# Kernel optimization log

Measured on AMD Instinct MI355X. Metric: run time of the kernel, lower is better.

Reference implementation:

```python
import jax, jax.numpy as jnp
import numpy as np

B, S, H, NH = 4, 2048, 1024, 16
HS = H // NH


def setup_inputs() -> dict:
    key = jax.random.key(0)
    ks = jax.random.split(key, 9)
    s = 0.02
    return {
        "x": jax.random.normal(ks[0], (B, S, H), dtype=jnp.float32),
        "Wq": jax.random.normal(ks[1], (H, H), dtype=jnp.float32) * s,
        "bq": jnp.zeros((H,), dtype=jnp.float32),
        "Wk": jax.random.normal(ks[2], (H, H), dtype=jnp.float32) * s,
        "bk": jnp.zeros((H,), dtype=jnp.float32),
        "Wv": jax.random.normal(ks[3], (H, H), dtype=jnp.float32) * s,
        "bv": jnp.zeros((H,), dtype=jnp.float32),
        "Wp": jax.random.normal(ks[4], (H, H), dtype=jnp.float32) * s,
        "bp": jnp.zeros((H,), dtype=jnp.float32),
    }


def _split_heads(t):
    # [B,S,H] -> [B,NH,S,HS]
    b, s, _ = t.shape
    return t.reshape(b, s, NH, HS).swapaxes(1, 2)


def reference(x, Wq, bq, Wk, bk, Wv, bv, Wp, bp):
    # torch Linear: y = x @ W.T + b
    q = _split_heads(x @ Wq.T + bq)
    k = _split_heads(x @ Wk.T + bk)
    v = _split_heads(x @ Wv.T + bv)
    scale = 1.0 / np.sqrt(HS).astype(np.float32)
    scores = jnp.einsum('bhqd,bhkd->bhqk', q, k) * scale  # [B,NH,S,S]
    n_pos = scores.shape[2]
    causal = jnp.arange(n_pos)[None, :] <= jnp.arange(n_pos)[:, None]
    mask_value = jnp.finfo(scores.dtype).min
    scores = jnp.where(causal, scores, mask_value)
    attn_w = jax.nn.softmax(scores, axis=-1)
    # dropout is identity in eval mode
    attn = jnp.einsum('bhqk,bhkd->bhqd', attn_w, v)
    attn = attn.swapaxes(1, 2).reshape(x.shape[0], n_pos, H)
    return attn @ Wp.T + bp
```

## Files before the change

kernel.cpp:

```cpp
#include <hip/hip_runtime.h>

#define B_ 4
#define S_ 2048
#define H_ 1024
#define NH_ 16
#define HS_ 64
#define SG_ (B_*S_)

typedef __bf16 bf16x8 __attribute__((ext_vector_type(8)));
typedef __bf16 bf16x4 __attribute__((ext_vector_type(4)));
typedef float  f32x4  __attribute__((ext_vector_type(4)));

#define M3(a,b,c) fmaxf(fmaxf((a),(b)),(c))

__device__ __forceinline__ void gload16(const void* g, void* l) {
    __builtin_amdgcn_global_load_lds(
        (const __attribute__((address_space(1))) void*)g,
        (__attribute__((address_space(3))) void*)l,
        16, 0, 0);
}

__global__ void cvt_f32_bf16(const float* __restrict__ in, __bf16* __restrict__ out, int n4) {
    int i = blockIdx.x * blockDim.x + threadIdx.x;
    if (i >= n4) return;
    float4 v = reinterpret_cast<const float4*>(in)[i];
    bf16x4 o;
    o[0] = (__bf16)v.x; o[1] = (__bf16)v.y; o[2] = (__bf16)v.z; o[3] = (__bf16)v.w;
    reinterpret_cast<bf16x4*>(out)[i] = o;
}

__global__ void cvt_w4(const float* __restrict__ w0, const float* __restrict__ w1,
                       const float* __restrict__ w2, const float* __restrict__ w3,
                       __bf16* __restrict__ o0, __bf16* __restrict__ o1,
                       __bf16* __restrict__ o2, __bf16* __restrict__ o3, int n4) {
    int i = blockIdx.x * blockDim.x + threadIdx.x;
    if (i >= n4) return;
    const float* in; __bf16* out;
    switch (blockIdx.y) {
        case 0: in = w0; out = o0; break;
        case 1: in = w1; out = o1; break;
        case 2: in = w2; out = o2; break;
        default: in = w3; out = o3; break;
    }
    float4 v = reinterpret_cast<const float4*>(in)[i];
    bf16x4 o;
    o[0] = (__bf16)v.x; o[1] = (__bf16)v.y; o[2] = (__bf16)v.z; o[3] = (__bf16)v.w;
    reinterpret_cast<bf16x4*>(out)[i] = o;
}

__device__ __forceinline__ void store_tile(const f32x4& acc, long mbase, long nbase, int lane,
                                           const float* __restrict__ bias, void* __restrict__ out,
                                           long N, int out_f32, int bias_row) {
    const int r16 = lane & 15, kg = lane >> 4;
    const long col = nbase + r16;
    const float bc = bias_row ? 0.f : bias[col];
#pragma unroll
    for (int r = 0; r < 4; ++r) {
        const long row = mbase + kg * 4 + r;
        const float v = acc[r] + (bias_row ? bias[row] : bc);
        if (out_f32) ((float*)out)[row * N + col] = v;
        else         ((__bf16*)out)[row * N + col] = (__bf16)v;
    }
}

__global__ __launch_bounds__(256) void gemm128(
    const __bf16* __restrict__ A, const __bf16* __restrict__ W,
    const float* __restrict__ bias, void* __restrict__ out,
    int M, int N, int K, int out_f32, int bias_row)
{
    __shared__ __bf16 sA[2][128][64];
    __shared__ __bf16 sB[2][128][64];
    const int lane = threadIdx.x & 63, widx = threadIdx.x >> 6;
    const int wr = widx >> 1, wc = widx & 1;
    const int c = lane & 15, g = lane >> 4;
    const long m0 = (long)blockIdx.y * 128, n0 = (long)blockIdx.x * 128;
    const int sr8 = lane >> 3;
    const int sc8 = lane & 7;

    auto STAGE = [&](int buf, int k0) {
#pragma unroll
        for (int it = 0; it < 4; ++it) {
            const int rb = it * 32 + widx * 8;
            const int row = rb + sr8;
            gload16(A + (m0 + row) * K + k0 + ((sc8 ^ (row & 7)) << 3), &sA[buf][rb][0]);
            gload16(W + (n0 + row) * K + k0 + ((sc8 ^ (row & 7)) << 3), &sB[buf][rb][0]);
        }
    };

    f32x4 acc[4][4] = {};

    STAGE(0, 0);
    __syncthreads();
    const int NK = K >> 6;
    for (int kt = 0; kt < NK; ++kt) {
        const int cur = kt & 1;
        if (kt + 1 < NK) STAGE(cur ^ 1, (kt + 1) << 6);

        bf16x8 af[2][4], bfr[2][4];
#pragma unroll
        for (int i = 0; i < 4; ++i) {
            const int ra = wr * 64 + i * 16 + c;
            const char* ap = (const char*)&sA[cur][ra][0];
            af[0][i] = *(const bf16x8*)(ap + ((( g    ) ^ (ra & 7)) << 4));
            af[1][i] = *(const bf16x8*)(ap + (((4 | g) ^ (ra & 7)) << 4));
            const int rbn = wc * 64 + i * 16 + c;
            const char* bp = (const char*)&sB[cur][rbn][0];
            bfr[0][i] = *(const bf16x8*)(bp + ((( g    ) ^ (rbn & 7)) << 4));
            bfr[1][i] = *(const bf16x8*)(bp + (((4 | g) ^ (rbn & 7)) << 4));
        }
#pragma unroll
        for (int kh = 0; kh < 2; ++kh)
#pragma unroll
            for (int i = 0; i < 4; ++i)
#pragma unroll
                for (int j = 0; j < 4; ++j)
                    acc[i][j] = __builtin_amdgcn_mfma_f32_16x16x32_bf16(af[kh][i], bfr[kh][j], acc[i][j], 0, 0, 0);
        __syncthreads();
    }

#pragma unroll
    for (int i = 0; i < 4; ++i)
#pragma unroll
        for (int j = 0; j < 4; ++j)
            store_tile(acc[i][j], m0 + wr * 64 + i * 16, n0 + wc * 64 + j * 16,
                       lane, bias, out, N, out_f32, bias_row);
}

__global__ __launch_bounds__(256) void attn_mfma2(
    const __bf16* __restrict__ Q, const __bf16* __restrict__ Kg,
    const __bf16* __restrict__ Vt, __bf16* __restrict__ Ab)
{
    __shared__ __bf16 ldsK[2][64][64];
    __shared__ __bf16 ldsV[2][64][64];
    __shared__ __bf16 ldsE[4][32 * 72];

    const int lane = threadIdx.x & 63, widx = threadIdx.x >> 6;
    const int c = lane & 15, g = lane >> 4;
    const int bid = blockIdx.x;
    const int bh = bid & 63, pi = bid >> 6;
    const int b = bh >> 4, h = bh & 15;

    const int sr8 = lane >> 3;
    const int sc8 = lane & 7;
    const float qscale = 0.125f * 1.4426950408889634f;

    auto STAGEKV = [&](int buf, int kt) {
#pragma unroll
        for (int it = 0; it < 2; ++it) {
            const int row = widx * 16 + it * 8 + sr8;
            gload16(Kg + ((long)(b * S_ + kt + row)) * H_ + h * HS_ + ((sc8 ^ (row & 7)) << 3),
                    &ldsK[buf][widx * 16 + it * 8][0]);
        }
#pragma unroll
        for (int it = 0; it < 2; ++it) {
            const int dr = widx * 16 + it * 8 + sr8;
            gload16(Vt + ((long)(h * HS_ + dr)) * SG_ + b * S_ + kt + ((sc8 ^ (dr & 7)) << 3),
                    &ldsV[buf][widx * 16 + it * 8][0]);
        }
    };

    for (int seg = 0; seg < 2; ++seg) {
        const int chunk = seg ? (15 - pi) : pi;
        const int q0w = chunk * 128 + widx * 32;

        bf16x8 qf[2][2];
#pragma unroll
        for (int qi = 0; qi < 2; ++qi)
#pragma unroll
            for (int hf = 0; hf < 2; ++hf) {
                const long qa = ((long)(b * S_ + q0w + qi * 16 + c)) * H_ + h * HS_ + hf * 32 + g * 8;
                bf16x8 t = *reinterpret_cast<const bf16x8*>(Q + qa);
#pragma unroll
                for (int j = 0; j < 8; ++j) t[j] = (__bf16)(qscale * (float)t[j]);
                qf[qi][hf] = t;
            }

        f32x4 ot[4][2] = {};
        float m[2] = {-1e30f, -1e30f}, l[2] = {0.f, 0.f};
        const int nt = 2 * (chunk + 1);

        STAGEKV(0, 0);
        __syncthreads();

        for (int t = 0; t < nt; ++t) {
            const int cur = t & 1;
            if (t + 1 < nt) STAGEKV(cur ^ 1, (t + 1) * 64);
            const int kt = t * 64;

            if (kt <= q0w + 31) {
                f32x4 st[4][2] = {};
#pragma unroll
                for (int t4 = 0; t4 < 4; ++t4) {
                    const int r = t4 * 16 + c;
                    const char* kp = (const char*)&ldsK[cur][r][0];
                    bf16x8 kf0 = *(const bf16x8*)(kp + (((g)     ^ (c & 7)) << 4));
                    bf16x8 kf1 = *(const bf16x8*)(kp + (((4 | g) ^ (c & 7)) << 4));
#pragma unroll
                    for (int qi = 0; qi < 2; ++qi) {
                        st[t4][qi] = __builtin_amdgcn_mfma_f32_16x16x32_bf16(kf0, qf[qi][0], st[t4][qi], 0, 0, 0);
                        st[t4][qi] = __builtin_amdgcn_mfma_f32_16x16x32_bf16(kf1, qf[qi][1], st[t4][qi], 0, 0, 0);
                    }
                }
                if (kt + 63 > q0w) {
#pragma unroll
                    for (int t4 = 0; t4 < 4; ++t4)
#pragma unroll
                        for (int qi = 0; qi < 2; ++qi)
#pragma unroll
                            for (int r = 0; r < 4; ++r)
                                if (kt + t4 * 16 + g * 4 + r > q0w + qi * 16 + c)
                                    st[t4][qi][r] = -1e30f;
                }
                bf16x8 pf[2][2];
                float fr[2];
                int resc = 0;
#pragma unroll
                for (int qi = 0; qi < 2; ++qi) {
                    const float a0 = M3(st[0][qi][0], st[0][qi][1], st[0][qi][2]);
                    const float a1 = M3(st[0][qi][3], st[1][qi][0], st[1][qi][1]);
                    const float a2 = M3(st[1][qi][2], st[1][qi][3], st[2][qi][0]);
                    const float a3 = M3(st[2][qi][1], st[2][qi][2], st[2][qi][3]);
                    const float a4 = M3(st[3][qi][0], st[3][qi][1], st[3][qi][2]);
                    float pm = M3(M3(a0, a1, a2), a3, fmaxf(a4, st[3][qi][3]));
                    pm = fmaxf(pm, __shfl_xor(pm, 16));
                    pm = fmaxf(pm, __shfl_xor(pm, 32));
                    const int defer = __all(pm - m[qi] <= 8.0f);
                    float mn;
                    if (defer) {
                        mn = m[qi]; fr[qi] = 1.0f;
                    } else {
                        mn = fmaxf(m[qi], pm);
                        fr[qi] = exp2f(m[qi] - mn);
                        m[qi] = mn;
                        resc = 1;
                    }
                    float p[16], rs = 0.f;
#pragma unroll
                    for (int t4 = 0; t4 < 4; ++t4)
#pragma unroll
                        for (int r = 0; r < 4; ++r) {
                            const float e = exp2f(st[t4][qi][r] - mn);
                            p[t4 * 4 + r] = e; rs += e;
                        }
                    rs += __shfl_xor(rs, 16);
                    rs += __shfl_xor(rs, 32);
                    l[qi] = l[qi] * fr[qi] + rs;
#pragma unroll
                    for (int j = 0; j < 8; ++j) {
                        pf[0][qi][j] = (__bf16)p[j];
                        pf[1][qi][j] = (__bf16)p[8 + j];
                    }
                }
                if (resc) {
#pragma unroll
                    for (int blk = 0; blk < 4; ++blk) {
                        ot[blk][0] *= fr[0];
                        ot[blk][1] *= fr[1];
                    }
                }
#pragma unroll
                for (int blk = 0; blk < 4; ++blk) {
                    const char* vp = (const char*)&ldsV[cur][blk * 16 + c][0];
                    const int sw = c & 7;
#pragma unroll
                    for (int hf = 0; hf < 2; ++hf) {
                        bf16x4 lo = *(const bf16x4*)(vp + ((((hf << 2) + (g >> 1))     ^ sw) << 4) + ((g & 1) << 3));
                        bf16x4 hi = *(const bf16x4*)(vp + ((((hf << 2) + 2 + (g >> 1)) ^ sw) << 4) + ((g & 1) << 3));
                        bf16x8 vf;
                        vf[0] = lo[0]; vf[1] = lo[1]; vf[2] = lo[2]; vf[3] = lo[3];
                        vf[4] = hi[0]; vf[5] = hi[1]; vf[6] = hi[2]; vf[7] = hi[3];
#pragma unroll
                        for (int qi = 0; qi < 2; ++qi)
                            ot[blk][qi] = __builtin_amdgcn_mfma_f32_16x16x32_bf16(vf, pf[hf][qi], ot[blk][qi], 0, 0, 0);
                    }
                }
            }
            __syncthreads();
        }

        __bf16* myo = ldsE[widx];
#pragma unroll
        for (int qi = 0; qi < 2; ++qi) {
            const float invl = 1.0f / l[qi];
#pragma unroll
            for (int blk = 0; blk < 4; ++blk) {
                bf16x4 tv;
#pragma unroll
                for (int r = 0; r < 4; ++r) tv[r] = (__bf16)(ot[blk][qi][r] * invl);
                *reinterpret_cast<bf16x4*>(myo + (qi * 16 + c) * 72 + blk * 16 + g * 4) = tv;
            }
        }
#pragma unroll
        for (int half = 0; half < 2; ++half) {
            const int qr = lane >> 2, dc = (lane & 3) * 16;
            const __bf16* src = myo + (half * 16 + qr) * 72 + dc;
            bf16x8 r0 = *reinterpret_cast<const bf16x8*>(src);
            bf16x8 r1 = *reinterpret_cast<const bf16x8*>(src + 8);
            __bf16* dst = Ab + ((long)(b * S_ + q0w + half * 16 + qr)) * H_ + h * HS_ + dc;
            *reinterpret_cast<bf16x8*>(dst) = r0;
            *reinterpret_cast<bf16x8*>(dst + 8) = r1;
        }
    }
}

extern "C" void kernel_launch(void* const* d_in, const int* in_sizes, int n_in,
                              void* d_out, int out_size, void* d_ws, size_t ws_size,
                              hipStream_t stream) {
    const float* x  = (const float*)d_in[0];
    const float* Wq = (const float*)d_in[1];
    const float* bq = (const float*)d_in[2];
    const float* Wk = (const float*)d_in[3];
    const float* bk = (const float*)d_in[4];
    const float* Wv = (const float*)d_in[5];
    const float* bv = (const float*)d_in[6];
    const float* Wp = (const float*)d_in[7];
    const float* bp = (const float*)d_in[8];
    float* out = (float*)d_out;

    const int M = SG_;
    const int N = H_;
    const int K = H_;

    char* ws = (char*)d_ws;
    size_t off = 0;
    __bf16* xb  = (__bf16*)(ws + off); off += (size_t)M * K * 2;
    __bf16* Wqb = (__bf16*)(ws + off); off += (size_t)N * K * 2;
    __bf16* Wkb = (__bf16*)(ws + off); off += (size_t)N * K * 2;
    __bf16* Wvb = (__bf16*)(ws + off); off += (size_t)N * K * 2;
    __bf16* Wpb = (__bf16*)(ws + off); off += (size_t)N * K * 2;
    __bf16* Qb  = (__bf16*)(ws + off); off += (size_t)M * H_ * 2;
    __bf16* Kbf = (__bf16*)(ws + off); off += (size_t)M * H_ * 2;
    __bf16* Vt  = (__bf16*)(ws + off); off += (size_t)M * H_ * 2;
    __bf16* Ab  = (__bf16*)(ws + off); off += (size_t)M * H_ * 2;

    {
        int n4 = M * K / 4;
        cvt_f32_bf16<<<(n4 + 255) / 256, 256, 0, stream>>>(x, xb, n4);
        int w4 = N * K / 4;
        dim3 gw((w4 + 255) / 256, 4);
        cvt_w4<<<gw, 256, 0, stream>>>(Wq, Wk, Wv, Wp, Wqb, Wkb, Wvb, Wpb, w4);
    }

    dim3 gg(N / 128, M / 128);
    gemm128<<<gg, 256, 0, stream>>>(xb, Wqb, bq, Qb,  M, N, K, 0, 0);
    gemm128<<<gg, 256, 0, stream>>>(xb, Wkb, bk, Kbf, M, N, K, 0, 0);
    dim3 gv(M / 128, N / 128);
    gemm128<<<gv, 256, 0, stream>>>(Wvb, xb, bv, Vt, N, M, K, 0, 1);

    attn_mfma2<<<512, 256, 0, stream>>>(Qb, Kbf, Vt, Ab);

    gemm128<<<gg, 256, 0, stream>>>(Ab, Wpb, bp, out, M, N, K, 1, 0);
}
```

Measured before the change: 306.9 us.

## Fuse QKV projections, add V transpose kernel, merge attention segments into one block

The three Q/K/V projections become a single GEMM launch over a 3072-wide output. The epilogue picks the bias and destination per 1024-column slice; this relies on the bf16 weight buffers sitting next to each other in the workspace. V is now written row-major and transposed by a new vtrans kernel into a permuted layout, so attention can read V fragments with single 16-byte LDS loads. Attention runs 512-thread blocks in which two wave groups process the paired causal chunks at the same time instead of one after the other, and the transposed V reuses the x buffer. The GEMM also drops double buffering and moves to 32-wide K tiles with a sync per step, which may cost latency hiding in the projections.

Result: faster. 290.3 us (-5.4%).

```diff
diff --git a/kernel.cpp b/kernel.cpp
--- a/kernel.cpp
+++ b/kernel.cpp
@@ -48,258 +48,265 @@
     reinterpret_cast<bf16x4*>(out)[i] = o;
 }
 
-__device__ __forceinline__ void store_tile(const f32x4& acc, long mbase, long nbase, int lane,
-                                           const float* __restrict__ bias, void* __restrict__ out,
-                                           long N, int out_f32, int bias_row) {
-    const int r16 = lane & 15, kg = lane >> 4;
-    const long col = nbase + r16;
-    const float bc = bias_row ? 0.f : bias[col];
-#pragma unroll
-    for (int r = 0; r < 4; ++r) {
-        const long row = mbase + kg * 4 + r;
-        const float v = acc[r] + (bias_row ? bias[row] : bc);
-        if (out_f32) ((float*)out)[row * N + col] = v;
-        else         ((__bf16*)out)[row * N + col] = (__bf16)v;
-    }
-}
-
 __global__ __launch_bounds__(256) void gemm128(
     const __bf16* __restrict__ A, const __bf16* __restrict__ W,
-    const float* __restrict__ bias, void* __restrict__ out,
-    int M, int N, int K, int out_f32, int bias_row)
+    const float* __restrict__ b0, const float* __restrict__ b1, const float* __restrict__ b2,
+    void* __restrict__ o0, void* __restrict__ o1, void* __restrict__ o2,
+    int K, int mode)
 {
-    __shared__ __bf16 sA[2][128][64];
-    __shared__ __bf16 sB[2][128][64];
+    __shared__ __bf16 sA[128][32];
+    __shared__ __bf16 sB[128][32];
     const int lane = threadIdx.x & 63, widx = threadIdx.x >> 6;
     const int wr = widx >> 1, wc = widx & 1;
     const int c = lane & 15, g = lane >> 4;
     const long m0 = (long)blockIdx.y * 128, n0 = (long)blockIdx.x * 128;
-    const int sr8 = lane >> 3;
-    const int sc8 = lane & 7;
-
-    auto STAGE = [&](int buf, int k0) {
-#pragma unroll
-        for (int it = 0; it < 4; ++it) {
-            const int rb = it * 32 + widx * 8;
-            const int row = rb + sr8;
-            gload16(A + (m0 + row) * K + k0 + ((sc8 ^ (row & 7)) << 3), &sA[buf][rb][0]);
-            gload16(W + (n0 + row) * K + k0 + ((sc8 ^ (row & 7)) << 3), &sB[buf][rb][0]);
-        }
-    };
+    const int srow = lane >> 2;
+    const int schunk = lane & 3;
 
     f32x4 acc[4][4] = {};
 
-    STAGE(0, 0);
-    __syncthreads();
-    const int NK = K >> 6;
-    for (int kt = 0; kt < NK; ++kt) {
-        const int cur = kt & 1;
-        if (kt + 1 < NK) STAGE(cur ^ 1, (kt + 1) << 6);
-
-        bf16x8 af[2][4], bfr[2][4];
+    for (int k0 = 0; k0 < K; k0 += 32) {
+#pragma unroll
+        for (int it = 0; it < 2; ++it) {
+            const int row = widx * 32 + it * 16 + srow;
+            gload16(A + (m0 + row) * K + k0 + ((schunk ^ (row & 3)) << 3),
+                    &sA[widx * 32 + it * 16][0]);
+            gload16(W + (n0 + row) * K + k0 + ((schunk ^ (row & 3)) << 3),
+                    &sB[widx * 32 + it * 16][0]);
+        }
+        __syncthreads();
+        bf16x8 af[4], bfr[4];
 #pragma unroll
         for (int i = 0; i < 4; ++i) {
             const int ra = wr * 64 + i * 16 + c;
-            const char* ap = (const char*)&sA[cur][ra][0];
-            af[0][i] = *(const bf16x8*)(ap + ((( g    ) ^ (ra & 7)) << 4));
-            af[1][i] = *(const bf16x8*)(ap + (((4 | g) ^ (ra & 7)) << 4));
-            const int rbn = wc * 64 + i * 16 + c;
-            const char* bp = (const char*)&sB[cur][rbn][0];
-            bfr[0][i] = *(const bf16x8*)(bp + ((( g    ) ^ (rbn & 7)) << 4));
-            bfr[1][i] = *(const bf16x8*)(bp + (((4 | g) ^ (rbn & 7)) << 4));
-        }
-#pragma unroll
-        for (int kh = 0; kh < 2; ++kh)
-#pragma unroll
-            for (int i = 0; i < 4; ++i)
-#pragma unroll
-                for (int j = 0; j < 4; ++j)
-                    acc[i][j] = __builtin_amdgcn_mfma_f32_16x16x32_bf16(af[kh][i], bfr[kh][j], acc[i][j], 0, 0, 0);
+            af[i]  = *(const bf16x8*)((const char*)&sA[ra][0] + ((g ^ (ra & 3)) << 4));
+            const int rb = wc * 64 + i * 16 + c;
+            bfr[i] = *(const bf16x8*)((const char*)&sB[rb][0] + ((g ^ (rb & 3)) << 4));
+        }
+#pragma unroll
+        for (int i = 0; i < 4; ++i)
+#pragma unroll
+            for (int j = 0; j < 4; ++j)
+                acc[i][j] = __builtin_amdgcn_mfma_f32_16x16x32_bf16(af[i], bfr[j], acc[i][j], 0, 0, 0);
         __syncthreads();
     }
 
+    const float* bias; void* ob; int obf16;
+    long ncl;
+    if (mode == 1) {
+        const int sel = (int)(n0 >> 10);
+        bias = sel == 0 ? b0 : (sel == 1 ? b1 : b2);
+        ob   = sel == 0 ? o0 : (sel == 1 ? o1 : o2);
+        ncl  = n0 & 1023; obf16 = 1;
+    } else {
+        bias = b0; ob = o0; ncl = n0; obf16 = 0;
+    }
 #pragma unroll
     for (int i = 0; i < 4; ++i)
 #pragma unroll
-        for (int j = 0; j < 4; ++j)
-            store_tile(acc[i][j], m0 + wr * 64 + i * 16, n0 + wc * 64 + j * 16,
-                       lane, bias, out, N, out_f32, bias_row);
-}
-
-__global__ __launch_bounds__(256) void attn_mfma2(
+        for (int j = 0; j < 4; ++j) {
+            const long col = ncl + wc * 64 + j * 16 + c;
+            const float bv = bias[col];
+#pragma unroll
+            for (int r = 0; r < 4; ++r) {
+                const long row = m0 + wr * 64 + i * 16 + g * 4 + r;
+                const float v = acc[i][j][r] + bv;
+                if (obf16) ((__bf16*)ob)[row * 1024 + col] = (__bf16)v;
+                else       ((float*)ob)[row * 1024 + col] = v;
+            }
+        }
+}
+
+__global__ __launch_bounds__(256) void vtrans(const __bf16* __restrict__ Vrow,
+                                              __bf16* __restrict__ Vt) {
+    __shared__ __bf16 tl[4][64][80];
+    const int lane = threadIdx.x & 63, w = threadIdx.x >> 6;
+    const int tile = blockIdx.x * 4 + w;
+    const int h = tile & 15;
+    const int sgg = (tile >> 4) << 6;
+    const int r8 = lane >> 3, c8 = lane & 7;
+#pragma unroll
+    for (int it = 0; it < 8; ++it) {
+        const int kv = it * 8 + r8;
+        bf16x8 v = *(const bf16x8*)(Vrow + (long)(sgg + kv) * H_ + h * 64 + c8 * 8);
+        *(bf16x8*)(&tl[w][kv][c8 * 8]) = v;
+    }
+    __syncthreads();
+    const int d = lane;
+#pragma unroll
+    for (int hf = 0; hf < 2; ++hf)
+#pragma unroll
+        for (int hi = 0; hi < 2; ++hi)
+#pragma unroll
+            for (int g4 = 0; g4 < 4; ++g4) {
+                const int kv = hf * 32 + hi * 16 + g4 * 4;
+                const int o  = hf * 32 + g4 * 8 + hi * 4;
+                bf16x4 t;
+#pragma unroll
+                for (int r = 0; r < 4; ++r) t[r] = tl[w][kv + r][d];
+                *(bf16x4*)(Vt + (long)(h * 64 + d) * SG_ + sgg + o) = t;
+            }
+}
+
+__global__ __launch_bounds__(512) void attn_mfma3(
     const __bf16* __restrict__ Q, const __bf16* __restrict__ Kg,
     const __bf16* __restrict__ Vt, __bf16* __restrict__ Ab)
 {
-    __shared__ __bf16 ldsK[2][64][64];
-    __shared__ __bf16 ldsV[2][64][64];
-    __shared__ __bf16 ldsE[4][32 * 72];
+    __shared__ char smem[38400];
+    __bf16 (*ldsK)[64][64] = (__bf16 (*)[64][64])smem;
+    __bf16 (*ldsV)[64][64] = (__bf16 (*)[64][64])(smem + 16384);
 
     const int lane = threadIdx.x & 63, widx = threadIdx.x >> 6;
     const int c = lane & 15, g = lane >> 4;
     const int bid = blockIdx.x;
     const int bh = bid & 63, pi = bid >> 6;
     const int b = bh >> 4, h = bh & 15;
+    const int chunk = (widx < 4) ? pi : (15 - pi);
+    const int q0w = chunk * 128 + (widx & 3) * 32;
 
     const int sr8 = lane >> 3;
     const int sc8 = lane & 7;
     const float qscale = 0.125f * 1.4426950408889634f;
 
+    bf16x8 qf[2][2];
+#pragma unroll
+    for (int qi = 0; qi < 2; ++qi)
+#pragma unroll
+        for (int hf = 0; hf < 2; ++hf) {
+            const long qa = ((long)(b * S_ + q0w + qi * 16 + c)) * H_ + h * HS_ + hf * 32 + g * 8;
+            bf16x8 t = *reinterpret_cast<const bf16x8*>(Q + qa);
+#pragma unroll
+            for (int j = 0; j < 8; ++j) t[j] = (__bf16)(qscale * (float)t[j]);
+            qf[qi][hf] = t;
+        }
+
+    f32x4 ot[4][2] = {};
+    float m[2] = {-1e30f, -1e30f}, l[2] = {0.f, 0.f};
+    const int NT = 32 - 2 * pi;
+
     auto STAGEKV = [&](int buf, int kt) {
-#pragma unroll
-        for (int it = 0; it < 2; ++it) {
-            const int row = widx * 16 + it * 8 + sr8;
-            gload16(Kg + ((long)(b * S_ + kt + row)) * H_ + h * HS_ + ((sc8 ^ (row & 7)) << 3),
-                    &ldsK[buf][widx * 16 + it * 8][0]);
-        }
-#pragma unroll
-        for (int it = 0; it < 2; ++it) {
-            const int dr = widx * 16 + it * 8 + sr8;
-            gload16(Vt + ((long)(h * HS_ + dr)) * SG_ + b * S_ + kt + ((sc8 ^ (dr & 7)) << 3),
-                    &ldsV[buf][widx * 16 + it * 8][0]);
-        }
+        const int row = widx * 8 + sr8;
+        gload16(Kg + ((long)(b * S_ + kt + row)) * H_ + h * HS_ + ((sc8 ^ (row & 7)) << 3),
+                &ldsK[buf][widx * 8][0]);
+        gload16(Vt + ((long)(h * HS_ + row)) * SG_ + b * S_ + kt + ((sc8 ^ (row & 7)) << 3),
+                &ldsV[buf][widx * 8][0]);
     };
 
-    for (int seg = 0; seg < 2; ++seg) {
-        const int chunk = seg ? (15 - pi) : pi;
-        const int q0w = chunk * 128 + widx * 32;
-
-        bf16x8 qf[2][2];
-#pragma unroll
-        for (int qi = 0; qi < 2; ++qi)
-#pragma unroll
-            for (int hf = 0; hf < 2; ++hf) {
-                const long qa = ((long)(b * S_ + q0w + qi * 16 + c)) * H_ + h * HS_ + hf * 32 + g * 8;
-                bf16x8 t = *reinterpret_cast<const bf16x8*>(Q + qa);
-#pragma unroll
-                for (int j = 0; j < 8; ++j) t[j] = (__bf16)(qscale * (float)t[j]);
-                qf[qi][hf] = t;
-            }
-
-        f32x4 ot[4][2] = {};
-        float m[2] = {-1e30f, -1e30f}, l[2] = {0.f, 0.f};
-        const int nt = 2 * (chunk + 1);
-
-        STAGEKV(0, 0);
+    STAGEKV(0, 0);
+    __syncthreads();
+
+    for (int t = 0; t < NT; ++t) {
+        const int cur = t & 1;
+        if (t + 1 < NT) STAGEKV(cur ^ 1, (t + 1) * 64);
+        const int kt = t * 64;
+
+        if (kt <= q0w + 31) {
+            f32x4 st[4][2] = {};
+#pragma unroll
+            for (int t4 = 0; t4 < 4; ++t4) {
+                const int r = t4 * 16 + c;
+                const char* kp = (const char*)&ldsK[cur][r][0];
+                bf16x8 kf0 = *(const bf16x8*)(kp + (((g)     ^ (c & 7)) << 4));
+                bf16x8 kf1 = *(const bf16x8*)(kp + (((4 | g) ^ (c & 7)) << 4));
+#pragma unroll
+                for (int qi = 0; qi < 2; ++qi) {
+                    st[t4][qi] = __builtin_amdgcn_mfma_f32_16x16x32_bf16(kf0, qf[qi][0], st[t4][qi], 0, 0, 0);
+                    st[t4][qi] = __builtin_amdgcn_mfma_f32_16x16x32_bf16(kf1, qf[qi][1], st[t4][qi], 0, 0, 0);
+                }
+            }
+            if (kt + 63 > q0w) {
+#pragma unroll
+                for (int t4 = 0; t4 < 4; ++t4)
+#pragma unroll
+                    for (int qi = 0; qi < 2; ++qi)
+#pragma unroll
+                        for (int r = 0; r < 4; ++r)
+                            if (kt + t4 * 16 + g * 4 + r > q0w + qi * 16 + c)
+                                st[t4][qi][r] = -1e30f;
+            }
+            bf16x8 pf[2][2];
+            float fr[2];
+            int resc = 0;
+#pragma unroll
+            for (int qi = 0; qi < 2; ++qi) {
+                const float a0 = M3(st[0][qi][0], st[0][qi][1], st[0][qi][2]);
+                const float a1 = M3(st[0][qi][3], st[1][qi][0], st[1][qi][1]);
+                const float a2 = M3(st[1][qi][2], st[1][qi][3], st[2][qi][0]);
+                const float a3 = M3(st[2][qi][1], st[2][qi][2], st[2][qi][3]);
+                const float a4 = M3(st[3][qi][0], st[3][qi][1], st[3][qi][2]);
+                float pm = M3(M3(a0, a1, a2), a3, fmaxf(a4, st[3][qi][3]));
+                pm = fmaxf(pm, __shfl_xor(pm, 16));
+                pm = fmaxf(pm, __shfl_xor(pm, 32));
+                const int defer = __all(pm - m[qi] <= 8.0f);
+                float mn;
+                if (defer) {
+                    mn = m[qi]; fr[qi] = 1.0f;
+                } else {
+                    mn = fmaxf(m[qi], pm);
+                    fr[qi] = exp2f(m[qi] - mn);
+                    m[qi] = mn;
+                    resc = 1;
+                }
+                float p[16], rs = 0.f;
+#pragma unroll
+                for (int t4 = 0; t4 < 4; ++t4)
+#pragma unroll
+                    for (int r = 0; r < 4; ++r) {
+                        const float e = exp2f(st[t4][qi][r] - mn);
+                        p[t4 * 4 + r] = e; rs += e;
+                    }
+                rs += __shfl_xor(rs, 16);
+                rs += __shfl_xor(rs, 32);
+                l[qi] = l[qi] * fr[qi] + rs;
+#pragma unroll
+                for (int j = 0; j < 8; ++j) {
+                    pf[0][qi][j] = (__bf16)p[j];
+                    pf[1][qi][j] = (__bf16)p[8 + j];
+                }
+            }
+            if (resc) {
+#pragma unroll
+                for (int blk = 0; blk < 4; ++blk) {
+                    ot[blk][0] *= fr[0];
+                    ot[blk][1] *= fr[1];
+                }
+            }
+#pragma unroll
+            for (int blk = 0; blk < 4; ++blk) {
+                const char* vp = (const char*)&ldsV[cur][blk * 16 + c][0];
+#pragma unroll
+                for (int hf = 0; hf < 2; ++hf) {
+                    bf16x8 vf = *(const bf16x8*)(vp + (((hf * 4 + g) ^ (c & 7)) << 4));
+#pragma unroll
+                    for (int qi = 0; qi < 2; ++qi)
+                        ot[blk][qi] = __builtin_amdgcn_mfma_f32_16x16x32_bf16(vf, pf[hf][qi], ot[blk][qi], 0, 0, 0);
+                }
+            }
+        }
         __syncthreads();
-
-        for (int t = 0; t < nt; ++t) {
-            const int cur = t & 1;
-            if (t + 1 < nt) STAGEKV(cur ^ 1, (t + 1) * 64);
-            const int kt = t * 64;
-
-            if (kt <= q0w + 31) {
-                f32x4 st[4][2] = {};
-#pragma unroll
-                for (int t4 = 0; t4 < 4; ++t4) {
-                    const int r = t4 * 16 + c;
-                    const char* kp = (const char*)&ldsK[cur][r][0];
-                    bf16x8 kf0 = *(const bf16x8*)(kp + (((g)     ^ (c & 7)) << 4));
-                    bf16x8 kf1 = *(const bf16x8*)(kp + (((4 | g) ^ (c & 7)) << 4));
-#pragma unroll
-                    for (int qi = 0; qi < 2; ++qi) {
-                        st[t4][qi] = __builtin_amdgcn_mfma_f32_16x16x32_bf16(kf0, qf[qi][0], st[t4][qi], 0, 0, 0);
-                        st[t4][qi] = __builtin_amdgcn_mfma_f32_16x16x32_bf16(kf1, qf[qi][1], st[t4][qi], 0, 0, 0);
-                    }
-                }
-                if (kt + 63 > q0w) {
-#pragma unroll
-                    for (int t4 = 0; t4 < 4; ++t4)
-#pragma unroll
-                        for (int qi = 0; qi < 2; ++qi)
-#pragma unroll
-                            for (int r = 0; r < 4; ++r)
-                                if (kt + t4 * 16 + g * 4 + r > q0w + qi * 16 + c)
-                                    st[t4][qi][r] = -1e30f;
-                }
-                bf16x8 pf[2][2];
-                float fr[2];
-                int resc = 0;
-#pragma unroll
-                for (int qi = 0; qi < 2; ++qi) {
-                    const float a0 = M3(st[0][qi][0], st[0][qi][1], st[0][qi][2]);
-                    const float a1 = M3(st[0][qi][3], st[1][qi][0], st[1][qi][1]);
-                    const float a2 = M3(st[1][qi][2], st[1][qi][3], st[2][qi][0]);
-                    const float a3 = M3(st[2][qi][1], st[2][qi][2], st[2][qi][3]);
-                    const float a4 = M3(st[3][qi][0], st[3][qi][1], st[3][qi][2]);
-                    float pm = M3(M3(a0, a1, a2), a3, fmaxf(a4, st[3][qi][3]));
-                    pm = fmaxf(pm, __shfl_xor(pm, 16));
-                    pm = fmaxf(pm, __shfl_xor(pm, 32));
-                    const int defer = __all(pm - m[qi] <= 8.0f);
-                    float mn;
-                    if (defer) {
-                        mn = m[qi]; fr[qi] = 1.0f;
-                    } else {
-                        mn = fmaxf(m[qi], pm);
-                        fr[qi] = exp2f(m[qi] - mn);
-                        m[qi] = mn;
-                        resc = 1;
-                    }
-                    float p[16], rs = 0.f;
-#pragma unroll
-                    for (int t4 = 0; t4 < 4; ++t4)
-#pragma unroll
-                        for (int r = 0; r < 4; ++r) {
-                            const float e = exp2f(st[t4][qi][r] - mn);
-                            p[t4 * 4 + r] = e; rs += e;
-                        }
-                    rs += __shfl_xor(rs, 16);
-                    rs += __shfl_xor(rs, 32);
-                    l[qi] = l[qi] * fr[qi] + rs;
-#pragma unroll
-                    for (int j = 0; j < 8; ++j) {
-                        pf[0][qi][j] = (__bf16)p[j];
-                        pf[1][qi][j] = (__bf16)p[8 + j];
-                    }
-                }
-                if (resc) {
-#pragma unroll
-                    for (int blk = 0; blk < 4; ++blk) {
-                        ot[blk][0] *= fr[0];
-                        ot[blk][1] *= fr[1];
-                    }
-                }
-#pragma unroll
-                for (int blk = 0; blk < 4; ++blk) {
-                    const char* vp = (const char*)&ldsV[cur][blk * 16 + c][0];
-                    const int sw = c & 7;
-#pragma unroll
-                    for (int hf = 0; hf < 2; ++hf) {
-                        bf16x4 lo = *(const bf16x4*)(vp + ((((hf << 2) + (g >> 1))     ^ sw) << 4) + ((g & 1) << 3));
-                        bf16x4 hi = *(const bf16x4*)(vp + ((((hf << 2) + 2 + (g >> 1)) ^ sw) << 4) + ((g & 1) << 3));
-                        bf16x8 vf;
-                        vf[0] = lo[0]; vf[1] = lo[1]; vf[2] = lo[2]; vf[3] = lo[3];
-                        vf[4] = hi[0]; vf[5] = hi[1]; vf[6] = hi[2]; vf[7] = hi[3];
-#pragma unroll
-                        for (int qi = 0; qi < 2; ++qi)
-                            ot[blk][qi] = __builtin_amdgcn_mfma_f32_16x16x32_bf16(vf, pf[hf][qi], ot[blk][qi], 0, 0, 0);
-                    }
-                }
-            }
-            __syncthreads();
-        }
-
-        __bf16* myo = ldsE[widx];
-#pragma unroll
-        for (int qi = 0; qi < 2; ++qi) {
-            const float invl = 1.0f / l[qi];
-#pragma unroll
-            for (int blk = 0; blk < 4; ++blk) {
-                bf16x4 tv;
-#pragma unroll
-                for (int r = 0; r < 4; ++r) tv[r] = (__bf16)(ot[blk][qi][r] * invl);
-                *reinterpret_cast<bf16x4*>(myo + (qi * 16 + c) * 72 + blk * 16 + g * 4) = tv;
-            }
-        }
-#pragma unroll
-        for (int half = 0; half < 2; ++half) {
-            const int qr = lane >> 2, dc = (lane & 3) * 16;
-            const __bf16* src = myo + (half * 16 + qr) * 72 + dc;
-            bf16x8 r0 = *reinterpret_cast<const bf16x8*>(src);
-            bf16x8 r1 = *reinterpret_cast<const bf16x8*>(src + 8);
-            __bf16* dst = Ab + ((long)(b * S_ + q0w + half * 16 + qr)) * H_ + h * HS_ + dc;
-            *reinterpret_cast<bf16x8*>(dst) = r0;
-            *reinterpret_cast<bf16x8*>(dst + 8) = r1;
-        }
+    }
+
+    __bf16* myo = (__bf16*)smem + widx * (32 * 72);
+#pragma unroll
+    for (int qi = 0; qi < 2; ++qi) {
+        const float invl = 1.0f / l[qi];
+#pragma unroll
+        for (int blk = 0; blk < 4; ++blk) {
+            bf16x4 tv;
+#pragma unroll
+            for (int r = 0; r < 4; ++r) tv[r] = (__bf16)(ot[blk][qi][r] * invl);
+            *reinterpret_cast<bf16x4*>(myo + (qi * 16 + c) * 72 + blk * 16 + g * 4) = tv;
+        }
+    }
+#pragma unroll
+    for (int half = 0; half < 2; ++half) {
+        const int qr = lane >> 2, dc = (lane & 3) * 16;
+        const __bf16* src = myo + (half * 16 + qr) * 72 + dc;
+        bf16x8 r0 = *reinterpret_cast<const bf16x8*>(src);
+        bf16x8 r1 = *reinterpret_cast<const bf16x8*>(src + 8);
+        __bf16* dst = Ab + ((long)(b * S_ + q0w + half * 16 + qr)) * H_ + h * HS_ + dc;
+        *reinterpret_cast<bf16x8*>(dst) = r0;
+        *reinterpret_cast<bf16x8*>(dst + 8) = r1;
     }
 }
 
@@ -318,36 +325,40 @@
     float* out = (float*)d_out;
 
     const int M = SG_;
-    const int N = H_;
     const int K = H_;
 
     char* ws = (char*)d_ws;
     size_t off = 0;
-    __bf16* xb  = (__bf16*)(ws + off); off += (size_t)M * K * 2;
-    __bf16* Wqb = (__bf16*)(ws + off); off += (size_t)N * K * 2;
-    __bf16* Wkb = (__bf16*)(ws + off); off += (size_t)N * K * 2;
-    __bf16* Wvb = (__bf16*)(ws + off); off += (size_t)N * K * 2;
-    __bf16* Wpb = (__bf16*)(ws + off); off += (size_t)N * K * 2;
-    __bf16* Qb  = (__bf16*)(ws + off); off += (size_t)M * H_ * 2;
-    __bf16* Kbf = (__bf16*)(ws + off); off += (size_t)M * H_ * 2;
-    __bf16* Vt  = (__bf16*)(ws + off); off += (size_t)M * H_ * 2;
-    __bf16* Ab  = (__bf16*)(ws + off); off += (size_t)M * H_ * 2;
+    __bf16* xb   = (__bf16*)(ws + off); off += (size_t)M * K * 2;
+    __bf16* Wqb  = (__bf16*)(ws + off); off += (size_t)H_ * K * 2;
+    __bf16* Wkb  = (__bf16*)(ws + off); off += (size_t)H_ * K * 2;
+    __bf16* Wvb  = (__bf16*)(ws + off); off += (size_t)H_ * K * 2;
+    __bf16* Wpb  = (__bf16*)(ws + off); off += (size_t)H_ * K * 2;
+    __bf16* Qb   = (__bf16*)(ws + off); off += (size_t)M * H_ * 2;
+    __bf16* Kbf  = (__bf16*)(ws + off); off += (size_t)M * H_ * 2;
+    __bf16* Vrow = (__bf16*)(ws + off); off += (size_t)M * H_ * 2;
+    __bf16* Ab   = (__bf16*)(ws + off); off += (size_t)M * H_ * 2;
+    __bf16* Vt   = xb;
 
     {
         int n4 = M * K / 4;
         cvt_f32_bf16<<<(n4 + 255) / 256, 256, 0, stream>>>(x, xb, n4);
-        int w4 = N * K / 4;
+        int w4 = H_ * K / 4;
         dim3 gw((w4 + 255) / 256, 4);
         cvt_w4<<<gw, 256, 0, stream>>>(Wq, Wk, Wv, Wp, Wqb, Wkb, Wvb, Wpb, w4);
     }
 
-    dim3 gg(N / 128, M / 128);
-    gemm128<<<gg, 256, 0, stream>>>(xb, Wqb, bq, Qb,  M, N, K, 0, 0);
-    gemm128<<<gg, 256, 0, stream>>>(xb, Wkb, bk, Kbf, M, N, K, 0, 0);
-    dim3 gv(M / 128, N / 128);
-    gemm128<<<gv, 256, 0, stream>>>(Wvb, xb, bv, Vt, N, M, K, 0, 1);
-
-    attn_mfma2<<<512, 256, 0, stream>>>(Qb, Kbf, Vt, Ab);
-
-    gemm128<<<gg, 256, 0, stream>>>(Ab, Wpb, bp, out, M, N, K, 1, 0);
-}
+    {
+        dim3 g(3 * H_ / 128, M / 128);
+        gemm128<<<g, 256, 0, stream>>>(xb, Wqb, bq, bk, bv, Qb, Kbf, Vrow, K, 1);
+    }
+
+    vtrans<<<512, 256, 0, stream>>>(Vrow, Vt);
+
+    attn_mfma3<<<512, 512, 0, stream>>>(Qb, Kbf, Vt, Ab);
+
+    {
+        dim3 g(H_ / 128, M / 128);
+        gemm128<<<g, 256, 0, stream>>>(Ab, Wpb, bp, nullptr, nullptr, out, nullptr, nullptr, K, 0);
+    }
+}
```
